# Kernel tuning notes

Hardware: AMD Instinct MI355X
Metric: run time of the kernel (lower is better)

## Reference

```python
import jax, jax.numpy as jnp
import numpy as np
import math

N_HEAD = 16

def setup_inputs() -> dict:
    key = jax.random.key(0)
    ks = jax.random.split(key, 5)
    B, T, C = 4, 2048, 1024
    return {
        "x": jax.random.normal(ks[0], (B, T, C), dtype=jnp.float32),
        "w_attn": jax.random.normal(ks[1], (3 * C, C), dtype=jnp.float32) * (1.0 / math.sqrt(C)),
        "b_attn": jax.random.normal(ks[2], (3 * C,), dtype=jnp.float32) * 0.02,
        "w_proj": jax.random.normal(ks[3], (C, C), dtype=jnp.float32) * (1.0 / math.sqrt(C)),
        "b_proj": jax.random.normal(ks[4], (C,), dtype=jnp.float32) * 0.02,
    }

def reference(x, w_attn, b_attn, w_proj, b_proj):
    B, T, C = x.shape
    H = N_HEAD
    hd = C // H
    # fused qkv projection: [B,T,3C]
    qkv = jnp.einsum('btc,fc->btf', x, w_attn) + b_attn
    q, k, v = jnp.split(qkv, 3, axis=-1)
    # [B,H,T,hd]
    q = q.reshape(B, T, H, hd).transpose(0, 2, 1, 3)
    k = k.reshape(B, T, H, hd).transpose(0, 2, 1, 3)
    v = v.reshape(B, T, H, hd).transpose(0, 2, 1, 3)
    scale = 1.0 / math.sqrt(hd)
    scores = jnp.einsum('bhqd,bhkd->bhqk', q, k) * scale  # [B,H,T,T]
    causal = jnp.tril(jnp.ones((T, T), dtype=bool))
    scores = jnp.where(causal, scores, jnp.finfo(scores.dtype).min)
    attn = jax.nn.softmax(scores, axis=-1)
    y = jnp.einsum('bhqk,bhkd->bhqd', attn, v)  # [B,H,T,hd]
    y = y.transpose(0, 2, 1, 3).reshape(B, T, C)
    return jnp.einsum('btc,oc->bto', y, w_proj) + b_proj
```

## Files before the change

kernel.cpp:

```cpp
#include <hip/hip_runtime.h>
#include <math.h>

typedef _Float16 f16;
typedef _Float16 __attribute__((ext_vector_type(8))) f16x8;
typedef _Float16 __attribute__((ext_vector_type(4))) f16x4;
typedef float __attribute__((ext_vector_type(4))) f32x4;
typedef float __attribute__((ext_vector_type(16))) f32x16;
typedef unsigned int u32;
typedef u32 __attribute__((ext_vector_type(4))) u32x4;

#define MFMA16(a, b, c) __builtin_amdgcn_mfma_f32_16x16x32_f16(a, b, c, 0, 0, 0)
#define MFMA32(a, b, c) __builtin_amdgcn_mfma_f32_32x32x16_f16(a, b, c, 0, 0, 0)

typedef const u32 __attribute__((address_space(1))) gas_u32;
typedef u32 __attribute__((address_space(3))) las_u32;

__device__ __forceinline__ void gload_lds16(const void* gptr, void* lptr) {
  unsigned long long gi = (unsigned long long)gptr;
  u32 li = (u32)(unsigned long long)lptr;
  __builtin_amdgcn_global_load_lds((gas_u32*)gi, (las_u32*)li, 16, 0, 0);
}

__device__ __forceinline__ u32 pkf16(float a, float b) {
  union { f16 h[2]; u32 u; } x;
  x.h[0] = (f16)a; x.h[1] = (f16)b;
  return x.u;
}

__global__ void castk(const float* __restrict__ in, f16* __restrict__ out, int n4) {
  int i = blockIdx.x * blockDim.x + threadIdx.x;
  if (i >= n4) return;
  float4 f = ((const float4*)in)[i];
  f16x4 h;
  h[0] = (f16)f.x; h[1] = (f16)f.y; h[2] = (f16)f.z; h[3] = (f16)f.w;
  *(f16x4*)(out + 4 * (size_t)i) = h;
}

__global__ __launch_bounds__(256) void vtrans(const f16* __restrict__ in,
                                              f16* __restrict__ out) {
  __shared__ __align__(16) f16 S[64 * 64];
  const int bh = blockIdx.y, t0 = blockIdx.x * 64;
  const int tid = threadIdx.x;
  const int r = tid >> 3;
  const int g = tid & 7;
#pragma unroll
  for (int h2 = 0; h2 < 2; ++h2) {
    const int row = r + 32 * h2;
    f16x8 v = *(const f16x8*)(in + ((size_t)bh * 2048 + t0 + row) * 64 + g * 8);
    *(f16x8*)&S[row * 64 + 8 * (g ^ (row & 7))] = v;
  }
  __syncthreads();
  f16* outt = out + (((size_t)bh * 32) + (t0 >> 6)) * 4096;
#pragma unroll
  for (int h2 = 0; h2 < 2; ++h2) {
    const int d = r + 32 * h2;
    f16x8 v;
#pragma unroll
    for (int j = 0; j < 8; ++j) {
      const int key = g * 8 + j;
      v[j] = S[key * 64 + 8 * ((d >> 3) ^ (key & 7)) + (d & 7)];
    }
    *(f16x8*)(outt + d * 64 + (g ^ (d & 7)) * 8) = v;
  }
}

template <int EPI>
__global__ __launch_bounds__(256) void gemm_bt(
    const f16* __restrict__ A, const f16* __restrict__ Bw,
    const float* __restrict__ bias,
    f16* __restrict__ Oq, f16* __restrict__ Ok, f16* __restrict__ Ov,
    float* __restrict__ Of,
    const int M, const int N, const int K) {
  __shared__ __align__(16) f16 As[128 * 32];
  __shared__ __align__(16) f16 Bs[128 * 32];
  const int tid = threadIdx.x;
  const int l = tid & 63;
  const int w = tid >> 6;
  const int wr = w >> 1, wc = w & 1;
  const int lr = l & 15, lg = l >> 4;
  const int nwg = gridDim.x * gridDim.y;
  const int idl = blockIdx.y * gridDim.x + blockIdx.x;
  const int id = (idl & 7) * (nwg >> 3) + (idl >> 3);
  const int m0 = (id / gridDim.x) * 128;
  const int n0 = (id % gridDim.x) * 128;

  const int srow = tid >> 2;
  const int scol = (tid & 3) * 8;

  f32x4 acc[4][4];
#pragma unroll
  for (int i = 0; i < 4; ++i)
#pragma unroll
    for (int j = 0; j < 4; ++j) acc[i][j] = (f32x4){0.f, 0.f, 0.f, 0.f};

  for (int k0 = 0; k0 < K; k0 += 32) {
    gload_lds16(A + (size_t)(m0 + srow) * K + k0 + scol, As + tid * 8);
    gload_lds16(A + (size_t)(m0 + srow + 64) * K + k0 + scol, As + 2048 + tid * 8);
    gload_lds16(Bw + (size_t)(n0 + srow) * K + k0 + scol, Bs + tid * 8);
    gload_lds16(Bw + (size_t)(n0 + srow + 64) * K + k0 + scol, Bs + 2048 + tid * 8);
    __syncthreads();

    f16x8 af[4], bfr[4];
#pragma unroll
    for (int i = 0; i < 4; ++i)
      af[i] = *(const f16x8*)&As[(wr * 64 + i * 16 + lr) * 32 + lg * 8];
#pragma unroll
    for (int j = 0; j < 4; ++j)
      bfr[j] = *(const f16x8*)&Bs[(wc * 64 + j * 16 + lr) * 32 + lg * 8];
#pragma unroll
    for (int i = 0; i < 4; ++i)
#pragma unroll
      for (int j = 0; j < 4; ++j) acc[i][j] = MFMA16(af[i], bfr[j], acc[i][j]);
    __syncthreads();
  }

#pragma unroll
  for (int i = 0; i < 4; ++i) {
    const int rbase = m0 + wr * 64 + i * 16 + lg * 4;
#pragma unroll
    for (int j = 0; j < 4; ++j) {
      const int col = n0 + wc * 64 + j * 16 + lr;
      const float bv = bias[col];
#pragma unroll
      for (int jj = 0; jj < 4; ++jj) {
        const int r = rbase + jj;
        const float val = acc[i][j][jj] + bv;
        if (EPI == 0) {
          Of[(size_t)r * N + col] = val;
        } else {
          const int which = col >> 10;
          const int inner = col & 1023;
          const int h = inner >> 6;
          int d = inner & 63;
          if (which == 1) d = (((d >> 3) ^ (r & 7)) << 3) | (d & 7);
          f16* dst = (which == 0) ? Oq : (which == 1) ? Ok : Ov;
          dst[(size_t)(((r >> 11) * 16 + h) * 2048 + (r & 2047)) * 64 + d] = (f16)val;
        }
      }
    }
  }
}

__global__ __launch_bounds__(256, 4) void attn_fwd(
    const f16* __restrict__ Qg, const f16* __restrict__ Kg,
    const f16* __restrict__ VPg, f16* __restrict__ Yg) {
  const int T = 2048;
  const int nwg = gridDim.x * gridDim.y;
  const int idl = blockIdx.y * gridDim.x + blockIdx.x;
  const int id = (idl & 7) * (nwg >> 3) + (idl >> 3);
  const int qt = id & 15;
  const int bh = id >> 4;
  const int q0 = qt * 128;
  const int tid = threadIdx.x;
  const int w = tid >> 6;
  const int l = tid & 63;
  const int l31 = l & 31;
  const int hi = l >> 5;
  const int qw0 = q0 + w * 32;
  const int qg = qw0 + l31;

  const f16* Qh = Qg + (size_t)bh * T * 64;
  const f16* Kh = Kg + (size_t)bh * T * 64;
  const f16* VPh = VPg + (size_t)bh * 32 * 4096;

  __shared__ __align__(16) f16 Ks[2][64 * 64];
  __shared__ __align__(16) f16 Vs[2][64 * 64];
  __shared__ float invs[4][32];

  const float SCL = 0.125f * 1.44269504088896f;

  f16x8 qf[4];
#pragma unroll
  for (int c = 0; c < 4; ++c) {
    f16x8 t = *(const f16x8*)(Qh + (size_t)qg * 64 + c * 16 + hi * 8);
#pragma unroll
    for (int j = 0; j < 8; ++j) t[j] = (f16)(SCL * (float)t[j]);
    qf[c] = t;
  }

  f32x16 acc0, acc1;
#pragma unroll
  for (int reg = 0; reg < 16; ++reg) { acc0[reg] = 0.f; acc1[reg] = 0.f; }
  float lsum = 0.f;

  const int off = (w * 16) * 64 + l * 8;

  gload_lds16(Kh + off, &Ks[0][off]);
  gload_lds16(Kh + 512 + off, &Ks[0][512 + off]);
  gload_lds16(VPh + off, &Vs[0][off]);
  gload_lds16(VPh + 512 + off, &Vs[0][512 + off]);

  const int nt = (q0 >> 6) + 2;
  for (int t = 0; t < nt; ++t) {
    __syncthreads();
    if (t + 1 < nt) {
      const int cur1 = (t + 1) & 1;
      const f16* Kt = Kh + (size_t)(t + 1) * 4096;
      const f16* Vt = VPh + (size_t)(t + 1) * 4096;
      gload_lds16(Kt + off, &Ks[cur1][off]);
      gload_lds16(Kt + 512 + off, &Ks[cur1][512 + off]);
      gload_lds16(Vt + off, &Vs[cur1][off]);
      gload_lds16(Vt + 512 + off, &Vs[cur1][512 + off]);
    }
    const int kb = t << 6;
    if (kb < qw0 + 32) {
      const f16* Kb = Ks[t & 1];
      const f16* Vb = Vs[t & 1];
      const bool dodiag = (kb + 64 > qw0);
#pragma unroll
      for (int H = 0; H < 2; ++H) {
        f32x16 S;
#pragma unroll
        for (int reg = 0; reg < 16; ++reg) S[reg] = 0.f;
        const int r = H * 32 + l31;
        const int r7 = r & 7;
#pragma unroll
        for (int c = 0; c < 4; ++c) {
          f16x8 kf = *(const f16x8*)(Kb + r * 64 + 8 * (((c << 1) + hi) ^ r7));
          S = MFMA32(kf, qf[c], S);
        }
        float p[16];
#pragma unroll
        for (int reg = 0; reg < 16; ++reg) {
          float s = S[reg];
          if (dodiag) {
            const int kgl = kb + H * 32 + ((reg & 3) + 8 * (reg >> 2) + 4 * hi);
            if (kgl > qg) s = -1e30f;
          }
          const float pv = exp2f(s - 8.0f);
          lsum += pv;
          p[reg] = pv;
        }
#pragma unroll
        for (int u = 0; u < 2; ++u) {
          const u32 P0 = pkf16(p[8 * u + 0], p[8 * u + 1]);
          const u32 P1 = pkf16(p[8 * u + 2], p[8 * u + 3]);
          const u32 P2 = pkf16(p[8 * u + 4], p[8 * u + 5]);
          const u32 P3 = pkf16(p[8 * u + 6], p[8 * u + 7]);
          const u32 X0 = __shfl_xor((int)P0, 32);
          const u32 X1 = __shfl_xor((int)P1, 32);
          const u32 X2 = __shfl_xor((int)P2, 32);
          const u32 X3 = __shfl_xor((int)P3, 32);
          u32x4 pw;
          pw[0] = hi ? X2 : P0;
          pw[1] = hi ? X3 : P1;
          pw[2] = hi ? P2 : X0;
          pw[3] = hi ? P3 : X1;
          const f16x8 pa = __builtin_bit_cast(f16x8, pw);
          const int up = ((2 * H + u) << 1) + hi;
          const f16x8 vf0 = *(const f16x8*)(Vb + l31 * 64 + 8 * (up ^ (l31 & 7)));
          const f16x8 vf1 = *(const f16x8*)(Vb + (32 + l31) * 64 + 8 * (up ^ ((32 + l31) & 7)));
          acc0 = MFMA32(pa, vf0, acc0);
          acc1 = MFMA32(pa, vf1, acc1);
        }
      }
    }
  }

  lsum += __shfl_xor(lsum, 32);
  if (hi == 0) invs[w][l31] = 1.f / lsum;
  const int bI = bh >> 4, hI = bh & 15;
#pragma unroll
  for (int reg = 0; reg < 16; ++reg) {
    const int row = (reg & 3) + 8 * (reg >> 2) + 4 * hi;
    const float iv = invs[w][row];
    f16* yp = Yg + (size_t)(bI * 2048 + qw0 + row) * 1024 + hI * 64;
    yp[l31] = (f16)(acc0[reg] * iv);
    yp[32 + l31] = (f16)(acc1[reg] * iv);
  }
}

extern "C" void kernel_launch(void* const* d_in, const int* in_sizes, int n_in,
                              void* d_out, int out_size, void* d_ws, size_t ws_size,
                              hipStream_t stream) {
  (void)in_sizes; (void)n_in; (void)out_size; (void)ws_size;
  const float* x      = (const float*)d_in[0];
  const float* w_attn = (const float*)d_in[1];
  const float* b_attn = (const float*)d_in[2];
  const float* w_proj = (const float*)d_in[3];
  const float* b_proj = (const float*)d_in[4];
  float* out = (float*)d_out;

  const int Bz = 4, T = 2048, Cc = 1024;
  const int M = Bz * T;

  f16* ws  = (f16*)d_ws;
  f16* wab = ws;
  f16* wpb = wab + (size_t)3 * Cc * Cc;
  f16* qb  = wpb + (size_t)Cc * Cc;
  f16* kb  = qb + (size_t)M * Cc;
  f16* vb  = kb + (size_t)M * Cc;
  f16* xb  = vb + (size_t)M * Cc;
  f16* vtb = xb + (size_t)M * Cc;

  castk<<<dim3((M * Cc / 4 + 255) / 256), 256, 0, stream>>>(x, xb, M * Cc / 4);
  castk<<<dim3((3 * Cc * Cc / 4 + 255) / 256), 256, 0, stream>>>(w_attn, wab, 3 * Cc * Cc / 4);
  castk<<<dim3((Cc * Cc / 4 + 255) / 256), 256, 0, stream>>>(w_proj, wpb, Cc * Cc / 4);

  gemm_bt<1><<<dim3(3 * Cc / 128, M / 128), 256, 0, stream>>>(
      xb, wab, b_attn, qb, kb, vb, nullptr, M, 3 * Cc, Cc);

  vtrans<<<dim3(T / 64, Bz * 16), 256, 0, stream>>>(vb, vtb);

  attn_fwd<<<dim3(T / 128, Bz * 16), 256, 0, stream>>>(qb, kb, vtb, xb);

  gemm_bt<0><<<dim3(Cc / 128, M / 128), 256, 0, stream>>>(
      xb, wpb, b_proj, nullptr, nullptr, nullptr, out, M, Cc, Cc);
}
```

Measured before the change: 344.1 us.

## Pair causal query tiles per workgroup and compute row sums via MFMA

The attention kernel now launches half as many workgroups, each processing two query tiles (pa and 15-pa) in sequence, which balances causal work across workgroups and groups heads by XCD. The softmax denominator is now accumulated with an extra MFMA against a ones vector instead of scalar adds, a lane shuffle and a shared-memory reciprocal table. The float-to-half packing switches to the packed round-toward-zero convert intrinsic. In exchange it adds one MFMA per PV step, slightly changes rounding of P, and halves grid parallelism.

```diff
diff --git a/kernel.cpp b/kernel.cpp
--- a/kernel.cpp
+++ b/kernel.cpp
@@ -2,6 +2,7 @@
 #include <math.h>
 
 typedef _Float16 f16;
+typedef __fp16 __attribute__((ext_vector_type(2))) fp16x2_raw;
 typedef _Float16 __attribute__((ext_vector_type(8))) f16x8;
 typedef _Float16 __attribute__((ext_vector_type(4))) f16x4;
 typedef float __attribute__((ext_vector_type(4))) f32x4;
@@ -21,10 +22,9 @@
   __builtin_amdgcn_global_load_lds((gas_u32*)gi, (las_u32*)li, 16, 0, 0);
 }
 
-__device__ __forceinline__ u32 pkf16(float a, float b) {
-  union { f16 h[2]; u32 u; } x;
-  x.h[0] = (f16)a; x.h[1] = (f16)b;
-  return x.u;
+__device__ __forceinline__ u32 pk2(float a, float b) {
+  fp16x2_raw t = __builtin_amdgcn_cvt_pkrtz(a, b);
+  return __builtin_bit_cast(u32, t);
 }
 
 __global__ void castk(const float* __restrict__ in, f16* __restrict__ out, int n4) {
@@ -145,19 +145,16 @@
     const f16* __restrict__ Qg, const f16* __restrict__ Kg,
     const f16* __restrict__ VPg, f16* __restrict__ Yg) {
   const int T = 2048;
-  const int nwg = gridDim.x * gridDim.y;
   const int idl = blockIdx.y * gridDim.x + blockIdx.x;
-  const int id = (idl & 7) * (nwg >> 3) + (idl >> 3);
-  const int qt = id & 15;
-  const int bh = id >> 4;
-  const int q0 = qt * 128;
+  const int xcd = idl & 7;
+  const int j = idl >> 3;
+  const int bh = xcd + 8 * (j & 7);
+  const int pa = j >> 3;
   const int tid = threadIdx.x;
   const int w = tid >> 6;
   const int l = tid & 63;
   const int l31 = l & 31;
   const int hi = l >> 5;
-  const int qw0 = q0 + w * 32;
-  const int qg = qw0 + l31;
 
   const f16* Qh = Qg + (size_t)bh * T * 64;
   const f16* Kh = Kg + (size_t)bh * T * 64;
@@ -165,108 +162,116 @@
 
   __shared__ __align__(16) f16 Ks[2][64 * 64];
   __shared__ __align__(16) f16 Vs[2][64 * 64];
-  __shared__ float invs[4][32];
 
   const float SCL = 0.125f * 1.44269504088896f;
-
-  f16x8 qf[4];
-#pragma unroll
-  for (int c = 0; c < 4; ++c) {
-    f16x8 t = *(const f16x8*)(Qh + (size_t)qg * 64 + c * 16 + hi * 8);
-#pragma unroll
-    for (int j = 0; j < 8; ++j) t[j] = (f16)(SCL * (float)t[j]);
-    qf[c] = t;
-  }
-
-  f32x16 acc0, acc1;
-#pragma unroll
-  for (int reg = 0; reg < 16; ++reg) { acc0[reg] = 0.f; acc1[reg] = 0.f; }
-  float lsum = 0.f;
-
   const int off = (w * 16) * 64 + l * 8;
 
-  gload_lds16(Kh + off, &Ks[0][off]);
-  gload_lds16(Kh + 512 + off, &Ks[0][512 + off]);
-  gload_lds16(VPh + off, &Vs[0][off]);
-  gload_lds16(VPh + 512 + off, &Vs[0][512 + off]);
-
-  const int nt = (q0 >> 6) + 2;
-  for (int t = 0; t < nt; ++t) {
+  f16x8 ones;
+#pragma unroll
+  for (int i2 = 0; i2 < 8; ++i2) ones[i2] = (f16)1.0f;
+
+  const int bI = bh >> 4, hI = bh & 15;
+
+#pragma unroll 1
+  for (int ph = 0; ph < 2; ++ph) {
+    const int qt = ph ? (15 - pa) : pa;
+    const int q0 = qt * 128;
+    const int qw0 = q0 + w * 32;
+    const int qg = qw0 + l31;
+
+    f16x8 qf[4];
+#pragma unroll
+    for (int c = 0; c < 4; ++c) {
+      f16x8 t = *(const f16x8*)(Qh + (size_t)qg * 64 + c * 16 + hi * 8);
+#pragma unroll
+      for (int jj = 0; jj < 8; ++jj) t[jj] = (f16)(SCL * (float)t[jj]);
+      qf[c] = t;
+    }
+
+    f32x16 acc0, acc1, accS;
+#pragma unroll
+    for (int reg = 0; reg < 16; ++reg) { acc0[reg] = 0.f; acc1[reg] = 0.f; accS[reg] = 0.f; }
+
     __syncthreads();
-    if (t + 1 < nt) {
-      const int cur1 = (t + 1) & 1;
-      const f16* Kt = Kh + (size_t)(t + 1) * 4096;
-      const f16* Vt = VPh + (size_t)(t + 1) * 4096;
-      gload_lds16(Kt + off, &Ks[cur1][off]);
-      gload_lds16(Kt + 512 + off, &Ks[cur1][512 + off]);
-      gload_lds16(Vt + off, &Vs[cur1][off]);
-      gload_lds16(Vt + 512 + off, &Vs[cur1][512 + off]);
-    }
-    const int kb = t << 6;
-    if (kb < qw0 + 32) {
-      const f16* Kb = Ks[t & 1];
-      const f16* Vb = Vs[t & 1];
-      const bool dodiag = (kb + 64 > qw0);
-#pragma unroll
-      for (int H = 0; H < 2; ++H) {
-        f32x16 S;
-#pragma unroll
-        for (int reg = 0; reg < 16; ++reg) S[reg] = 0.f;
-        const int r = H * 32 + l31;
-        const int r7 = r & 7;
-#pragma unroll
-        for (int c = 0; c < 4; ++c) {
-          f16x8 kf = *(const f16x8*)(Kb + r * 64 + 8 * (((c << 1) + hi) ^ r7));
-          S = MFMA32(kf, qf[c], S);
-        }
-        float p[16];
-#pragma unroll
-        for (int reg = 0; reg < 16; ++reg) {
-          float s = S[reg];
-          if (dodiag) {
-            const int kgl = kb + H * 32 + ((reg & 3) + 8 * (reg >> 2) + 4 * hi);
-            if (kgl > qg) s = -1e30f;
+    gload_lds16(Kh + off, &Ks[0][off]);
+    gload_lds16(Kh + 512 + off, &Ks[0][512 + off]);
+    gload_lds16(VPh + off, &Vs[0][off]);
+    gload_lds16(VPh + 512 + off, &Vs[0][512 + off]);
+
+    const int nt = (q0 >> 6) + 2;
+    for (int t = 0; t < nt; ++t) {
+      __syncthreads();
+      if (t + 1 < nt) {
+        const int cur1 = (t + 1) & 1;
+        const f16* Kt = Kh + (size_t)(t + 1) * 4096;
+        const f16* Vt = VPh + (size_t)(t + 1) * 4096;
+        gload_lds16(Kt + off, &Ks[cur1][off]);
+        gload_lds16(Kt + 512 + off, &Ks[cur1][512 + off]);
+        gload_lds16(Vt + off, &Vs[cur1][off]);
+        gload_lds16(Vt + 512 + off, &Vs[cur1][512 + off]);
+      }
+      const int kb = t << 6;
+      if (kb < qw0 + 32) {
+        const f16* Kb = Ks[t & 1];
+        const f16* Vb = Vs[t & 1];
+        const bool dodiag = (kb + 64 > qw0);
+#pragma unroll
+        for (int H = 0; H < 2; ++H) {
+          f32x16 S;
+#pragma unroll
+          for (int reg = 0; reg < 16; ++reg) S[reg] = 0.f;
+          const int r = H * 32 + l31;
+          const int r7 = r & 7;
+#pragma unroll
+          for (int c = 0; c < 4; ++c) {
+            f16x8 kf = *(const f16x8*)(Kb + r * 64 + 8 * (((c << 1) + hi) ^ r7));
+            S = MFMA32(kf, qf[c], S);
           }
-          const float pv = exp2f(s - 8.0f);
-          lsum += pv;
-          p[reg] = pv;
-        }
-#pragma unroll
-        for (int u = 0; u < 2; ++u) {
-          const u32 P0 = pkf16(p[8 * u + 0], p[8 * u + 1]);
-          const u32 P1 = pkf16(p[8 * u + 2], p[8 * u + 3]);
-          const u32 P2 = pkf16(p[8 * u + 4], p[8 * u + 5]);
-          const u32 P3 = pkf16(p[8 * u + 6], p[8 * u + 7]);
-          const u32 X0 = __shfl_xor((int)P0, 32);
-          const u32 X1 = __shfl_xor((int)P1, 32);
-          const u32 X2 = __shfl_xor((int)P2, 32);
-          const u32 X3 = __shfl_xor((int)P3, 32);
-          u32x4 pw;
-          pw[0] = hi ? X2 : P0;
-          pw[1] = hi ? X3 : P1;
-          pw[2] = hi ? P2 : X0;
-          pw[3] = hi ? P3 : X1;
-          const f16x8 pa = __builtin_bit_cast(f16x8, pw);
-          const int up = ((2 * H + u) << 1) + hi;
-          const f16x8 vf0 = *(const f16x8*)(Vb + l31 * 64 + 8 * (up ^ (l31 & 7)));
-          const f16x8 vf1 = *(const f16x8*)(Vb + (32 + l31) * 64 + 8 * (up ^ ((32 + l31) & 7)));
-          acc0 = MFMA32(pa, vf0, acc0);
-          acc1 = MFMA32(pa, vf1, acc1);
+          float p[16];
+#pragma unroll
+          for (int reg = 0; reg < 16; ++reg) {
+            float s = S[reg];
+            if (dodiag) {
+              const int kgl = kb + H * 32 + ((reg & 3) + 8 * (reg >> 2) + 4 * hi);
+              if (kgl > qg) s = -1e30f;
+            }
+            p[reg] = exp2f(s - 8.0f);
+          }
+#pragma unroll
+          for (int u = 0; u < 2; ++u) {
+            const u32 P0 = pk2(p[8 * u + 0], p[8 * u + 1]);
+            const u32 P1 = pk2(p[8 * u + 2], p[8 * u + 3]);
+            const u32 P2 = pk2(p[8 * u + 4], p[8 * u + 5]);
+            const u32 P3 = pk2(p[8 * u + 6], p[8 * u + 7]);
+            const u32 X0 = __shfl_xor((int)P0, 32);
+            const u32 X1 = __shfl_xor((int)P1, 32);
+            const u32 X2 = __shfl_xor((int)P2, 32);
+            const u32 X3 = __shfl_xor((int)P3, 32);
+            u32x4 pw;
+            pw[0] = hi ? X2 : P0;
+            pw[1] = hi ? X3 : P1;
+            pw[2] = hi ? P2 : X0;
+            pw[3] = hi ? P3 : X1;
+            const f16x8 pfr = __builtin_bit_cast(f16x8, pw);
+            const int up = ((2 * H + u) << 1) + hi;
+            const f16x8 vf0 = *(const f16x8*)(Vb + l31 * 64 + 8 * (up ^ (l31 & 7)));
+            const f16x8 vf1 = *(const f16x8*)(Vb + (32 + l31) * 64 + 8 * (up ^ ((32 + l31) & 7)));
+            acc0 = MFMA32(pfr, vf0, acc0);
+            acc1 = MFMA32(pfr, vf1, acc1);
+            accS = MFMA32(pfr, ones, accS);
+          }
         }
       }
     }
-  }
-
-  lsum += __shfl_xor(lsum, 32);
-  if (hi == 0) invs[w][l31] = 1.f / lsum;
-  const int bI = bh >> 4, hI = bh & 15;
-#pragma unroll
-  for (int reg = 0; reg < 16; ++reg) {
-    const int row = (reg & 3) + 8 * (reg >> 2) + 4 * hi;
-    const float iv = invs[w][row];
-    f16* yp = Yg + (size_t)(bI * 2048 + qw0 + row) * 1024 + hI * 64;
-    yp[l31] = (f16)(acc0[reg] * iv);
-    yp[32 + l31] = (f16)(acc1[reg] * iv);
+
+#pragma unroll
+    for (int reg = 0; reg < 16; ++reg) {
+      const int row = (reg & 3) + 8 * (reg >> 2) + 4 * hi;
+      const float iv = 1.f / accS[reg];
+      f16* yp = Yg + (size_t)(bI * 2048 + qw0 + row) * 1024 + hI * 64;
+      yp[l31] = (f16)(acc0[reg] * iv);
+      yp[32 + l31] = (f16)(acc1[reg] * iv);
+    }
   }
 }
 
@@ -302,7 +307,7 @@
 
   vtrans<<<dim3(T / 64, Bz * 16), 256, 0, stream>>>(vb, vtb);
 
-  attn_fwd<<<dim3(T / 128, Bz * 16), 256, 0, stream>>>(qb, kb, vtb, xb);
+  attn_fwd<<<dim3(8, Bz * 16), 256, 0, stream>>>(qb, kb, vtb, xb);
 
   gemm_bt<0><<<dim3(Cc / 128, M / 128), 256, 0, stream>>>(
       xb, wpb, b_proj, nullptr, nullptr, nullptr, out, M, Cc, Cc);
```

Measured after the change: 309.4 us. -10.1%, faster.
